# Kernel tuning notes

Measured on AMD Instinct MI355X. Metric: run time of the kernel, lower is better.

## Reference

```python
import jax, jax.numpy as jnp
import numpy as np

N, E, B = 50000, 400000, 64
N_INC, E_OUTC, U_INC, G_INC = 64, 64, 32, 64
H1A, H1B = 128, 64           # node_model_mlp1_hidden_sizes
H2 = 256                     # node_model_mlp2_hidden_sizes[0]
DIM_LH, DIM_L, N_OUTC = 128, 32, 64
LN_EPS = 1e-5

def _lin_init(key, din, dout):
    k1, k2 = jax.random.split(key)
    bound = 1.0 / np.sqrt(din)
    W = jax.random.uniform(k1, (din, dout), jnp.float32, -bound, bound)
    b = jax.random.uniform(k2, (dout,), jnp.float32, -bound, bound)
    return W, b

def setup_inputs() -> dict:
    key = jax.random.key(0)
    ks = jax.random.split(key, 16)
    x = jax.random.normal(ks[0], (N, N_INC), jnp.float32)
    edge_index = jax.random.randint(ks[1], (2, E), 0, N, jnp.int64)
    edge_attr = jax.random.normal(ks[2], (E, E_OUTC), jnp.float32)
    u = jax.random.normal(ks[3], (B, U_INC), jnp.float32)
    batch = jnp.sort(jax.random.randint(ks[4], (N,), 0, B, jnp.int64))
    goal = jax.random.normal(ks[5], (N, G_INC), jnp.float32)
    W1, b1 = _lin_init(ks[6], N_INC + E_OUTC, H1A)
    g1, be1 = jnp.ones((H1A,), jnp.float32), jnp.zeros((H1A,), jnp.float32)
    W2, b2 = _lin_init(ks[7], H1A, H1B)
    mlp2_inc = N_INC + H1B + U_INC
    W3, b3 = _lin_init(ks[8], mlp2_inc, H2)
    g3, be3 = jnp.ones((H2,), jnp.float32), jnp.zeros((H2,), jnp.float32)
    W4, b4 = _lin_init(ks[9], H2, DIM_LH)
    g4, be4 = jnp.ones((DIM_LH,), jnp.float32), jnp.zeros((DIM_LH,), jnp.float32)
    Wm, bm = _lin_init(ks[10], DIM_LH, DIM_L)
    Wv, bv = _lin_init(ks[11], DIM_LH, DIM_L)
    Wx, bx = _lin_init(ks[12], DIM_L, N_OUTC)
    return dict(x=x, edge_index=edge_index, edge_attr=edge_attr, u=u, batch=batch,
                goal=goal, W1=W1, b1=b1, g1=g1, be1=be1, W2=W2, b2=b2,
                W3=W3, b3=b3, g3=g3, be3=be3, W4=W4, b4=b4, g4=g4, be4=be4,
                Wm=Wm, bm=bm, Wv=Wv, bv=bv, Wx=Wx, bx=bx)

def _layernorm(h, g, b):
    mu = jnp.mean(h, axis=-1, keepdims=True)
    var = jnp.var(h, axis=-1, keepdims=True)
    return (h - mu) * jax.lax.rsqrt(var + LN_EPS) * g + b

def reference(x, edge_index, edge_attr, u, batch, goal,
              W1, b1, g1, be1, W2, b2,
              W3, b3, g3, be3, W4, b4, g4, be4,
              Wm, bm, Wv, bv, Wx, bx):
    row, col = edge_index[0], edge_index[1]
    # --- edge MLP: gather x[row], concat edge_attr, 2-layer MLP with LN+ReLU
    se = jnp.concatenate([x[row], edge_attr], axis=1)          # [E, n_inc+e_outc]
    h = jax.nn.relu(_layernorm(se @ W1 + b1, g1, be1)) @ W2 + b2  # [E, H1B]
    # --- scatter_mean over destination nodes
    sums = jax.ops.segment_sum(h, col, num_segments=N)          # [N, H1B]
    cnts = jax.ops.segment_sum(jnp.ones((E,), h.dtype), col, num_segments=N)
    aggs = sums / jnp.maximum(cnts, 1.0)[:, None]
    # --- node MLP 2
    z = jnp.concatenate([x, aggs, u[batch]], axis=1)            # [N, mlp2_inc]
    z = jax.nn.relu(_layernorm(z @ W3 + b3, g3, be3))
    z = jax.nn.relu(_layernorm(z @ W4 + b4, g4, be4))           # [N, DIM_LH]
    z_mu = z @ Wm + bm
    z_var = z @ Wv + bv                                         # log-variance
    eps = jax.random.normal(jax.random.key(42), z_mu.shape, z_mu.dtype)
    z_s = z_mu + eps * jnp.exp(0.5 * z_var)                     # reparameterize
    out = z_s @ Wx + bx                                         # [N, n_outc]
    return (out, z_mu, z_var)
```

## Files before the change

### kernel.cpp

```cpp
#include <hip/hip_runtime.h>

#define NN 50000
#define EE 400000
#define NB 49

typedef __attribute__((ext_vector_type(8))) short bf16x8;
typedef __attribute__((ext_vector_type(4))) float f32x4;

__device__ __forceinline__ void fma4(float4& a, float s, const float4& w){
  a.x = fmaf(s, w.x, a.x);
  a.y = fmaf(s, w.y, a.y);
  a.z = fmaf(s, w.z, a.z);
  a.w = fmaf(s, w.w, a.w);
}

__device__ __forceinline__ unsigned short f2bf(float f){
  unsigned u = __float_as_uint(f);
  unsigned r = (u + 0x7fffu + ((u >> 16) & 1u)) >> 16;
  return (unsigned short)r;
}

__device__ __forceinline__ bf16x8 cvt8(float4 lo, float4 hi){
  bf16x8 r;
  r[0]=(short)f2bf(lo.x); r[1]=(short)f2bf(lo.y); r[2]=(short)f2bf(lo.z); r[3]=(short)f2bf(lo.w);
  r[4]=(short)f2bf(hi.x); r[5]=(short)f2bf(hi.y); r[6]=(short)f2bf(hi.z); r[7]=(short)f2bf(hi.w);
  return r;
}

__device__ __forceinline__ unsigned packhl(float v){
  unsigned hi = f2bf(v);
  float fh = __uint_as_float(hi << 16);
  unsigned lo = f2bf(v - fh);
  return (hi << 16) | lo;
}

__device__ __forceinline__ uint4 pack4(float4 v){
  uint4 p;
  p.x = packhl(v.x); p.y = packhl(v.y); p.z = packhl(v.z); p.w = packhl(v.w);
  return p;
}

__device__ __forceinline__ void unpack8(uint4 p0, uint4 p1, bf16x8& hi, bf16x8& lo){
  hi[0]=(short)(p0.x>>16); lo[0]=(short)(p0.x & 0xffffu);
  hi[1]=(short)(p0.y>>16); lo[1]=(short)(p0.y & 0xffffu);
  hi[2]=(short)(p0.z>>16); lo[2]=(short)(p0.z & 0xffffu);
  hi[3]=(short)(p0.w>>16); lo[3]=(short)(p0.w & 0xffffu);
  hi[4]=(short)(p1.x>>16); lo[4]=(short)(p1.x & 0xffffu);
  hi[5]=(short)(p1.y>>16); lo[5]=(short)(p1.y & 0xffffu);
  hi[6]=(short)(p1.z>>16); lo[6]=(short)(p1.z & 0xffffu);
  hi[7]=(short)(p1.w>>16); lo[7]=(short)(p1.w & 0xffffu);
}

__device__ __forceinline__ float blo(unsigned u){ return __uint_as_float(u << 16); }
__device__ __forceinline__ float bhi(unsigned u){ return __uint_as_float(u & 0xffff0000u); }

__device__ __forceinline__ unsigned rotl32(unsigned v, int d){ return (v<<d)|(v>>(32-d)); }

__device__ __forceinline__ float eps_at(unsigned idx){
  const unsigned k0 = 0u, k1 = 42u, k2 = 0x1BD11BDAu ^ 0u ^ 42u;
  unsigned x0 = 0u + k0, x1 = idx + k1;
  const int rotA[4] = {13,15,26,6};
  const int rotB[4] = {17,29,16,24};
  #pragma unroll
  for (int i=0;i<4;i++){ x0 += x1; x1 = rotl32(x1, rotA[i]); x1 ^= x0; }
  x0 += k1; x1 += k2 + 1u;
  #pragma unroll
  for (int i=0;i<4;i++){ x0 += x1; x1 = rotl32(x1, rotB[i]); x1 ^= x0; }
  x0 += k2; x1 += k0 + 2u;
  #pragma unroll
  for (int i=0;i<4;i++){ x0 += x1; x1 = rotl32(x1, rotA[i]); x1 ^= x0; }
  x0 += k0; x1 += k1 + 3u;
  #pragma unroll
  for (int i=0;i<4;i++){ x0 += x1; x1 = rotl32(x1, rotB[i]); x1 ^= x0; }
  x0 += k1; x1 += k2 + 4u;
  #pragma unroll
  for (int i=0;i<4;i++){ x0 += x1; x1 = rotl32(x1, rotA[i]); x1 ^= x0; }
  x0 += k2; x1 += k0 + 5u;
  unsigned bits = x0 ^ x1;
  float f = __uint_as_float((bits >> 9) | 0x3f800000u) - 1.0f;
  const float lo = -0.99999994f;
  float u = f * 2.0f + lo;
  u = fmaxf(u, lo);
  float w = -log1pf(-u*u);
  float p;
  if (w < 5.0f){
    w -= 2.5f;
    p = 2.81022636e-08f;
    p = fmaf(p,w, 3.43273939e-07f);
    p = fmaf(p,w,-3.5233877e-06f);
    p = fmaf(p,w,-4.39150654e-06f);
    p = fmaf(p,w, 0.00021858087f);
    p = fmaf(p,w,-0.00125372503f);
    p = fmaf(p,w,-0.00417768164f);
    p = fmaf(p,w, 0.246640727f);
    p = fmaf(p,w, 1.50140941f);
  } else {
    w = sqrtf(w) - 3.0f;
    p = -0.000200214257f;
    p = fmaf(p,w, 0.000100950558f);
    p = fmaf(p,w, 0.00134934322f);
    p = fmaf(p,w,-0.00367342844f);
    p = fmaf(p,w, 0.00573950773f);
    p = fmaf(p,w,-0.0076224613f);
    p = fmaf(p,w, 0.00943887047f);
    p = fmaf(p,w, 1.00167406f);
    p = fmaf(p,w, 2.83297682f);
  }
  return 1.41421356237f * (p * u);
}

__global__ __launch_bounds__(256) void k_prep_x(const float* __restrict__ x,
                                                unsigned short* __restrict__ xb){
  int t = blockIdx.x*256 + threadIdx.x;
  if (t < NN*64/8){
    const float4* p = (const float4*)(x + t*8);
    bf16x8 v = cvt8(p[0], p[1]);
    *(bf16x8*)(xb + t*8) = v;
  }
}

__global__ __launch_bounds__(256) void k_prep_w(const float* __restrict__ W1,
                                                const float* __restrict__ W2,
                                                unsigned short* __restrict__ W1T,
                                                unsigned short* __restrict__ W2T){
  for (int i = threadIdx.x; i < 128*128; i += 256){
    int n = i >> 7, k = i & 127;
    W1T[i] = f2bf(W1[k*128 + n]);
  }
  for (int i = threadIdx.x; i < 64*128; i += 256){
    int n = i >> 7, k = i & 127;
    W2T[i] = f2bf(W2[k*64 + n]);
  }
}

__global__ __launch_bounds__(256) void k_prep_w34(const float* __restrict__ W3,
                                                  const float* __restrict__ W4,
                                                  unsigned short* __restrict__ W3Th,
                                                  unsigned short* __restrict__ W3Tl,
                                                  unsigned short* __restrict__ W4Th,
                                                  unsigned short* __restrict__ W4Tl){
  int b = blockIdx.x;
  if (b < 256){
    int n = b;
    for (int k = threadIdx.x; k < 160; k += 256){
      float w = W3[k*256 + n];
      unsigned h = f2bf(w);
      float fh = __uint_as_float(h << 16);
      W3Th[n*160 + k] = (unsigned short)h;
      W3Tl[n*160 + k] = f2bf(w - fh);
    }
  } else {
    int n = b - 256;
    int k = threadIdx.x;
    float w = W4[k*128 + n];
    unsigned h = f2bf(w);
    float fh = __uint_as_float(h << 16);
    W4Th[n*256 + k] = (unsigned short)h;
    W4Tl[n*256 + k] = f2bf(w - fh);
  }
}

__global__ __launch_bounds__(256) void k_hist(const int* __restrict__ ei, int* __restrict__ cnt){
  int e = blockIdx.x*256 + threadIdx.x;
  if (e < EE) atomicAdd(&cnt[ei[EE + e]], 1);
}

__global__ __launch_bounds__(256) void k_scan1(const int* __restrict__ cnt,
                                               int* __restrict__ offs,
                                               int* __restrict__ partials){
  __shared__ int sdata[256];
  const int t = threadIdx.x, b = blockIdx.x;
  const int base = b*1024 + t*4;
  int v0 = (base+0 < NN) ? cnt[base+0] : 0;
  int v1 = (base+1 < NN) ? cnt[base+1] : 0;
  int v2 = (base+2 < NN) ? cnt[base+2] : 0;
  int v3 = (base+3 < NN) ? cnt[base+3] : 0;
  int tsum = v0+v1+v2+v3;
  sdata[t] = tsum;
  __syncthreads();
  for (int off=1; off<256; off<<=1){
    int add = (t >= off) ? sdata[t-off] : 0;
    __syncthreads();
    sdata[t] += add;
    __syncthreads();
  }
  int run = sdata[t] - tsum;
  if (base+0 < NN) offs[base+0] = run;  run += v0;
  if (base+1 < NN) offs[base+1] = run;  run += v1;
  if (base+2 < NN) offs[base+2] = run;  run += v2;
  if (base+3 < NN) offs[base+3] = run;
  if (t == 255) partials[b] = sdata[255];
}

__global__ __launch_bounds__(64) void k_scan2(int* __restrict__ partials){
  int l = threadIdx.x;
  int v = (l < NB) ? partials[l] : 0;
  int inc = v;
  #pragma unroll
  for (int off=1; off<64; off<<=1){
    int t = __shfl_up(inc, off);
    if (l >= off) inc += t;
  }
  if (l < NB) partials[l] = inc - v;
}

__global__ __launch_bounds__(256) void k_scan3(int* __restrict__ offs,
                                               const int* __restrict__ partials,
                                               int* __restrict__ cursor){
  const int t = threadIdx.x, b = blockIdx.x;
  const int base = b*1024 + t*4;
  int add = partials[b];
  #pragma unroll
  for (int k=0;k<4;k++){
    int i = base + k;
    if (i < NN){ int o = offs[i] + add; offs[i] = o; cursor[i] = o; }
  }
}

__global__ __launch_bounds__(256) void k_fill(const int* __restrict__ ei,
                                              int* __restrict__ cursor,
                                              int* __restrict__ epos){
  int e = blockIdx.x*256 + threadIdx.x;
  if (e < EE){
    int c = ei[EE + e];
    epos[e] = atomicAdd(&cursor[c], 1);
  }
}

#define H1STR 132
__global__ __launch_bounds__(256, 4) void k_edge(const int* __restrict__ ei,
    const float* __restrict__ ea,
    const unsigned short* __restrict__ xb,
    const unsigned short* __restrict__ W1T, const float* __restrict__ b1,
    const float* __restrict__ g1, const float* __restrict__ be1,
    const unsigned short* __restrict__ W2T, const float* __restrict__ b2,
    const int* __restrict__ epos,
    unsigned short* __restrict__ h_ws){
  __shared__ __align__(16) float h1[64*H1STR];
  __shared__ int rows_l[64];
  __shared__ int slot_l[64];
  const int tid  = threadIdx.x;
  const int base = blockIdx.x * 64;
  const int wv   = tid >> 6;
  const int lane = tid & 63;
  const int quad = lane >> 4;
  const int l16  = lane & 15;
  if (tid < 64) rows_l[tid] = ei[base + tid];
  if (tid >= 128 && tid < 192) slot_l[tid-128] = epos[base + tid - 128];
  __syncthreads();
  {
    int rw[4];
    #pragma unroll
    for (int m=0;m<4;m++) rw[m] = rows_l[m*16 + l16];
    f32x4 acc[4][2];
    #pragma unroll
    for (int m=0;m<4;m++){ acc[m][0] = (f32x4){0.f,0.f,0.f,0.f}; acc[m][1] = (f32x4){0.f,0.f,0.f,0.f}; }
    #pragma unroll
    for (int ks=0; ks<4; ks++){
      bf16x8 af[4];
      if (ks < 2){
        #pragma unroll
        for (int m=0;m<4;m++)
          af[m] = *(const bf16x8*)(xb + (size_t)rw[m]*64 + ks*32 + quad*8);
      } else {
        #pragma unroll
        for (int m=0;m<4;m++){
          const float* p = ea + (size_t)(base + m*16 + l16)*64 + (ks-2)*32 + quad*8;
          af[m] = cvt8(*(const float4*)p, *(const float4*)(p+4));
        }
      }
      bf16x8 bf0 = *(const bf16x8*)(W1T + (size_t)((2*wv+0)*16 + l16)*128 + ks*32 + quad*8);
      bf16x8 bf1 = *(const bf16x8*)(W1T + (size_t)((2*wv+1)*16 + l16)*128 + ks*32 + quad*8);
      #pragma unroll
      for (int m=0;m<4;m++){
        acc[m][0] = __builtin_amdgcn_mfma_f32_16x16x32_bf16(af[m], bf0, acc[m][0], 0, 0, 0);
        acc[m][1] = __builtin_amdgcn_mfma_f32_16x16x32_bf16(af[m], bf1, acc[m][1], 0, 0, 0);
      }
    }
    #pragma unroll
    for (int nl=0; nl<2; nl++){
      float b1c = b1[(2*wv+nl)*16 + l16];
      #pragma unroll
      for (int m=0;m<4;m++){
        #pragma unroll
        for (int r=0;r<4;r++)
          h1[(m*16 + quad*4 + r)*H1STR + (2*wv+nl)*16 + l16] = acc[m][nl][r] + b1c;
      }
    }
  }
  __syncthreads();
  {
    const float gA = g1[lane], gB = g1[lane+64];
    const float bA = be1[lane], bB = be1[lane+64];
    for (int r = wv*16; r < wv*16 + 16; ++r){
      float a = h1[r*H1STR + lane];
      float b = h1[r*H1STR + 64 + lane];
      float s = a + b, ss = fmaf(a,a,b*b);
      #pragma unroll
      for (int off=32; off; off>>=1){
        s  += __shfl_xor(s, off);
        ss += __shfl_xor(ss, off);
      }
      float mean = s * (1.0f/128.0f);
      float var  = ss * (1.0f/128.0f) - mean*mean;
      float inv = rsqrtf(var + 1e-5f);
      h1[r*H1STR + lane]      = fmaxf(fmaf((a-mean)*inv, gA, bA), 0.f);
      h1[r*H1STR + 64 + lane] = fmaxf(fmaf((b-mean)*inv, gB, bB), 0.f);
    }
  }
  __syncthreads();
  {
    f32x4 acc2[4];
    #pragma unroll
    for (int m=0;m<4;m++) acc2[m] = (f32x4){0.f,0.f,0.f,0.f};
    #pragma unroll
    for (int ks=0; ks<4; ks++){
      bf16x8 bfr = *(const bf16x8*)(W2T + (size_t)(wv*16 + l16)*128 + ks*32 + quad*8);
      #pragma unroll
      for (int m=0;m<4;m++){
        const float* p = h1 + (m*16 + l16)*H1STR + ks*32 + quad*8;
        bf16x8 af = cvt8(*(const float4*)p, *(const float4*)(p+4));
        acc2[m] = __builtin_amdgcn_mfma_f32_16x16x32_bf16(af, bfr, acc2[m], 0, 0, 0);
      }
    }
    float b2c = b2[wv*16 + l16];
    #pragma unroll
    for (int m=0;m<4;m++){
      #pragma unroll
      for (int r=0;r<4;r++)
        h_ws[(size_t)slot_l[m*16 + quad*4 + r]*64 + wv*16 + l16] = f2bf(acc2[m][r] + b2c);
    }
  }
}

__global__ __launch_bounds__(256, 8) void k_agg(const float* __restrict__ x,
    const float* __restrict__ u, const int* __restrict__ batch,
    const unsigned short* __restrict__ h_ws, const int* __restrict__ cnt,
    const int* __restrict__ offs, unsigned* __restrict__ zg){
  int t = blockIdx.x*256 + threadIdx.x;
  int n = t >> 3, p = t & 7;
  if (n >= NN) return;
  unsigned* zr = zg + (size_t)n*160;
  {
    const float4* xp = (const float4*)(x + (size_t)n*64 + p*8);
    *(uint4*)(zr + p*8)     = pack4(xp[0]);
    *(uint4*)(zr + p*8 + 4) = pack4(xp[1]);
  }
  {
    const float4* up = (const float4*)(u + (size_t)batch[n]*32 + p*4);
    *(uint4*)(zr + 128 + p*4) = pack4(up[0]);
  }
  float a0=0.f,a1=0.f,a2=0.f,a3=0.f,a4=0.f,a5=0.f,a6=0.f,a7=0.f;
  int deg = cnt[n];
  const unsigned short* hp = h_ws + (size_t)offs[n]*64 + p*8;
  int j = 0;
  for (; j + 4 <= deg; j += 4){
    uint4 v0 = *(const uint4*)(hp);
    uint4 v1 = *(const uint4*)(hp + 64);
    uint4 v2 = *(const uint4*)(hp + 128);
    uint4 v3 = *(const uint4*)(hp + 192);
    hp += 256;
    a0 += blo(v0.x); a1 += bhi(v0.x); a2 += blo(v0.y); a3 += bhi(v0.y);
    a4 += blo(v0.z); a5 += bhi(v0.z); a6 += blo(v0.w); a7 += bhi(v0.w);
    a0 += blo(v1.x); a1 += bhi(v1.x); a2 += blo(v1.y); a3 += bhi(v1.y);
    a4 += blo(v1.z); a5 += bhi(v1.z); a6 += blo(v1.w); a7 += bhi(v1.w);
    a0 += blo(v2.x); a1 += bhi(v2.x); a2 += blo(v2.y); a3 += bhi(v2.y);
    a4 += blo(v2.z); a5 += bhi(v2.z); a6 += blo(v2.w); a7 += bhi(v2.w);
    a0 += blo(v3.x); a1 += bhi(v3.x); a2 += blo(v3.y); a3 += bhi(v3.y);
    a4 += blo(v3.z); a5 += bhi(v3.z); a6 += blo(v3.w); a7 += bhi(v3.w);
  }
  for (; j < deg; ++j){
    uint4 v = *(const uint4*)(hp);
    hp += 64;
    a0 += blo(v.x); a1 += bhi(v.x); a2 += blo(v.y); a3 += bhi(v.y);
    a4 += blo(v.z); a5 += bhi(v.z); a6 += blo(v.w); a7 += bhi(v.w);
  }
  float rc = 1.0f / fmaxf((float)deg, 1.0f);
  *(uint4*)(zr + 64 + p*8)     = pack4(make_float4(a0*rc, a1*rc, a2*rc, a3*rc));
  *(uint4*)(zr + 64 + p*8 + 4) = pack4(make_float4(a4*rc, a5*rc, a6*rc, a7*rc));
}

#define T2STR 132
#define ZSSTR 36
#define H3STR 260
__global__ __launch_bounds__(128, 3) void k_node(const unsigned* __restrict__ zg,
    const unsigned short* __restrict__ W3Th, const unsigned short* __restrict__ W3Tl,
    const float* __restrict__ b3,
    const float* __restrict__ g3, const float* __restrict__ be3,
    const unsigned short* __restrict__ W4Th, const unsigned short* __restrict__ W4Tl,
    const float* __restrict__ b4,
    const float* __restrict__ g4, const float* __restrict__ be4,
    const float* __restrict__ Wm, const float* __restrict__ bm,
    const float* __restrict__ Wv, const float* __restrict__ bv,
    const float* __restrict__ Wx, const float* __restrict__ bx,
    float* __restrict__ out){
  __shared__ __align__(16) char arena[(16*H3STR + 16*T2STR)*4];
  float*    h3f = (float*)arena;
  unsigned* h3p = (unsigned*)arena;
  float*    t2S = (float*)(arena + 16*H3STR*4);

  const int tid = threadIdx.x;
  const int base = blockIdx.x * 16;
  const int wv   = tid >> 6;
  const int lane = tid & 63;
  const int quad = lane >> 4;
  const int l16  = lane & 15;

  {
    const unsigned* az = zg + (size_t)(base + l16)*160 + quad*8;
    f32x4 acc[8];
    #pragma unroll
    for (int i=0;i<8;i++) acc[i] = (f32x4){0.f,0.f,0.f,0.f};
    #pragma unroll
    for (int ks=0; ks<5; ks++){
      uint4 p0 = *(const uint4*)(az + ks*32);
      uint4 p1 = *(const uint4*)(az + ks*32 + 4);
      bf16x8 ah, al;
      unpack8(p0, p1, ah, al);
      #pragma unroll
      for (int i=0;i<8;i++){
        int nt = wv*8 + i;
        bf16x8 bh = *(const bf16x8*)(W3Th + (size_t)(nt*16 + l16)*160 + ks*32 + quad*8);
        bf16x8 bl = *(const bf16x8*)(W3Tl + (size_t)(nt*16 + l16)*160 + ks*32 + quad*8);
        acc[i] = __builtin_amdgcn_mfma_f32_16x16x32_bf16(ah, bh, acc[i], 0, 0, 0);
        acc[i] = __builtin_amdgcn_mfma_f32_16x16x32_bf16(al, bh, acc[i], 0, 0, 0);
        acc[i] = __builtin_amdgcn_mfma_f32_16x16x32_bf16(ah, bl, acc[i], 0, 0, 0);
      }
    }
    #pragma unroll
    for (int i=0;i<8;i++){
      int nt = wv*8 + i;
      float bc = b3[nt*16 + l16];
      #pragma unroll
      for (int r=0;r<4;r++)
        h3f[(quad*4 + r)*H3STR + nt*16 + l16] = acc[i][r] + bc;
    }
  }
  __syncthreads();
  {
    float4 gg  = *(const float4*)(g3 + lane*4);
    float4 bet = *(const float4*)(be3 + lane*4);
    #pragma unroll
    for (int r=0;r<8;r++){
      int row = wv*8 + r;
      float4 v = *(const float4*)(h3f + row*H3STR + lane*4);
      float s  = v.x + v.y + v.z + v.w;
      float ss = fmaf(v.x,v.x, fmaf(v.y,v.y, fmaf(v.z,v.z, v.w*v.w)));
      #pragma unroll
      for (int off=32; off; off>>=1){ s += __shfl_xor(s,off); ss += __shfl_xor(ss,off); }
      float mean = s * (1.0f/256.0f);
      float inv  = rsqrtf(ss*(1.0f/256.0f) - mean*mean + 1e-5f);
      float4 o;
      o.x = fmaxf(fmaf((v.x-mean)*inv, gg.x, bet.x), 0.f);
      o.y = fmaxf(fmaf((v.y-mean)*inv, gg.y, bet.y), 0.f);
      o.z = fmaxf(fmaf((v.z-mean)*inv, gg.z, bet.z), 0.f);
      o.w = fmaxf(fmaf((v.w-mean)*inv, gg.w, bet.w), 0.f);
      *(uint4*)(h3p + row*H3STR + lane*4) = pack4(o);
    }
  }
  __syncthreads();
  {
    f32x4 acc[4];
    #pragma unroll
    for (int i=0;i<4;i++) acc[i] = (f32x4){0.f,0.f,0.f,0.f};
    #pragma unroll
    for (int ks=0; ks<8; ks++){
      const unsigned* ap = h3p + l16*H3STR + ks*32 + quad*8;
      uint4 p0 = *(const uint4*)ap;
      uint4 p1 = *(const uint4*)(ap + 4);
      bf16x8 ah, al;
      unpack8(p0, p1, ah, al);
      #pragma unroll
      for (int i=0;i<4;i++){
        int nt = wv*4 + i;
        bf16x8 bh = *(const bf16x8*)(W4Th + (size_t)(nt*16 + l16)*256 + ks*32 + quad*8);
        bf16x8 bl = *(const bf16x8*)(W4Tl + (size_t)(nt*16 + l16)*256 + ks*32 + quad*8);
        acc[i] = __builtin_amdgcn_mfma_f32_16x16x32_bf16(ah, bh, acc[i], 0, 0, 0);
        acc[i] = __builtin_amdgcn_mfma_f32_16x16x32_bf16(al, bh, acc[i], 0, 0, 0);
        acc[i] = __builtin_amdgcn_mfma_f32_16x16x32_bf16(ah, bl, acc[i], 0, 0, 0);
      }
    }
    #pragma unroll
    for (int i=0;i<4;i++){
      int nt = wv*4 + i;
      float bc = b4[nt*16 + l16];
      #pragma unroll
      for (int r=0;r<4;r++)
        t2S[(quad*4 + r)*T2STR + nt*16 + l16] = acc[i][r] + bc;
    }
  }
  __syncthreads();
  {
    const int jq = tid & 31, rb = tid >> 5;
    float4 gg  = *(const float4*)(g4 + 4*jq);
    float4 bet = *(const float4*)(be4 + 4*jq);
    #pragma unroll
    for (int r=0;r<4;r++){
      int row = rb*4 + r;
      float4 v = *(const float4*)(t2S + row*T2STR + 4*jq);
      float s  = v.x + v.y + v.z + v.w;
      float ss = fmaf(v.x,v.x, fmaf(v.y,v.y, fmaf(v.z,v.z, v.w*v.w)));
      #pragma unroll
      for (int off=16; off; off>>=1){ s += __shfl_xor(s,off); ss += __shfl_xor(ss,off); }
      float mean = s * (1.0f/128.0f);
      float inv  = rsqrtf(ss*(1.0f/128.0f) - mean*mean + 1e-5f);
      float4 o;
      o.x = fmaxf(fmaf((v.x-mean)*inv, gg.x, bet.x), 0.f);
      o.y = fmaxf(fmaf((v.y-mean)*inv, gg.y, bet.y), 0.f);
      o.z = fmaxf(fmaf((v.z-mean)*inv, gg.z, bet.z), 0.f);
      o.w = fmaxf(fmaf((v.w-mean)*inv, gg.w, bet.w), 0.f);
      *(float4*)(t2S + row*T2STR + 4*jq) = o;
    }
  }
  __syncthreads();
  {
    const int jq = tid & 15, rb = tid >> 4;
    const float* Wp = (jq < 8) ? Wm : Wv;
    const int cq = (jq & 7) * 4;
    float4 acc[2];
    #pragma unroll
    for (int r=0;r<2;r++) acc[r] = make_float4(0.f,0.f,0.f,0.f);
    #pragma unroll 2
    for (int k=0;k<128;k+=4){
      float4 w0 = *(const float4*)(Wp + (k+0)*32 + cq);
      float4 w1 = *(const float4*)(Wp + (k+1)*32 + cq);
      float4 w2 = *(const float4*)(Wp + (k+2)*32 + cq);
      float4 w3 = *(const float4*)(Wp + (k+3)*32 + cq);
      #pragma unroll
      for (int r=0;r<2;r++){
        float4 z = *(const float4*)(t2S + (rb*2+r)*T2STR + k);
        fma4(acc[r], z.x, w0); fma4(acc[r], z.y, w1);
        fma4(acc[r], z.z, w2); fma4(acc[r], z.w, w3);
      }
    }
    const float* bp = (jq < 8) ? bm : bv;
    float4 bb = *(const float4*)(bp + cq);
    const long long sec = (jq < 8) ? (long long)NN*64 : ((long long)NN*64 + (long long)NN*32);
    #pragma unroll
    for (int r=0;r<2;r++){
      float4 v = acc[r];
      v.x += bb.x; v.y += bb.y; v.z += bb.z; v.w += bb.w;
      int rr = rb*2 + r;
      *(float4*)(h3f + rr*64 + ((jq<8)?0:32) + cq) = v;
      int n = base + rr;
      if (n < NN) *(float4*)(out + sec + (long long)n*32 + cq) = v;
    }
  }
  __syncthreads();
  #pragma unroll
  for (int i=0;i<4;i++){
    int l = tid + 128*i;
    int r = l >> 5, jj = l & 31;
    float mu = h3f[r*64 + jj];
    float lv = h3f[r*64 + 32 + jj];
    unsigned idx = (unsigned)((base + r)*32 + jj);
    float e = eps_at(idx);
    t2S[r*ZSSTR + jj] = fmaf(e, expf(0.5f*lv), mu);
  }
  __syncthreads();
  {
    const int jq = tid & 15, rb = tid >> 4;
    float4 acc[2];
    #pragma unroll
    for (int r=0;r<2;r++) acc[r] = make_float4(0.f,0.f,0.f,0.f);
    #pragma unroll
    for (int k=0;k<32;k+=4){
      float4 w0 = *(const float4*)(Wx + (k+0)*64 + 4*jq);
      float4 w1 = *(const float4*)(Wx + (k+1)*64 + 4*jq);
      float4 w2 = *(const float4*)(Wx + (k+2)*64 + 4*jq);
      float4 w3 = *(const float4*)(Wx + (k+3)*64 + 4*jq);
      #pragma unroll
      for (int r=0;r<2;r++){
        float4 z = *(const float4*)(t2S + (rb*2+r)*ZSSTR + k);
        fma4(acc[r], z.x, w0); fma4(acc[r], z.y, w1);
        fma4(acc[r], z.z, w2); fma4(acc[r], z.w, w3);
      }
    }
    float4 bb = *(const float4*)(bx + 4*jq);
    #pragma unroll
    for (int r=0;r<2;r++){
      int n = base + rb*2 + r;
      if (n < NN){
        float4 v = acc[r];
        v.x += bb.x; v.y += bb.y; v.z += bb.z; v.w += bb.w;
        *(float4*)(out + (long long)n*64 + 4*jq) = v;
      }
    }
  }
}

extern "C" void kernel_launch(void* const* d_in, const int* in_sizes, int n_in,
                              void* d_out, int out_size, void* d_ws, size_t ws_size,
                              hipStream_t stream) {
  const float* x     = (const float*)d_in[0];
  const int*   ei    = (const int*)d_in[1];
  const float* ea    = (const float*)d_in[2];
  const float* u     = (const float*)d_in[3];
  const int*   batch = (const int*)d_in[4];
  const float* W1 = (const float*)d_in[6];
  const float* b1 = (const float*)d_in[7];
  const float* g1 = (const float*)d_in[8];
  const float* be1= (const float*)d_in[9];
  const float* W2 = (const float*)d_in[10];
  const float* b2 = (const float*)d_in[11];
  const float* W3 = (const float*)d_in[12];
  const float* b3 = (const float*)d_in[13];
  const float* g3 = (const float*)d_in[14];
  const float* be3= (const float*)d_in[15];
  const float* W4 = (const float*)d_in[16];
  const float* b4 = (const float*)d_in[17];
  const float* g4 = (const float*)d_in[18];
  const float* be4= (const float*)d_in[19];
  const float* Wm = (const float*)d_in[20];
  const float* bm = (const float*)d_in[21];
  const float* Wv = (const float*)d_in[22];
  const float* bv = (const float*)d_in[23];
  const float* Wx = (const float*)d_in[24];
  const float* bx = (const float*)d_in[25];

  char* W = (char*)d_ws;
  size_t off = 0;
  unsigned short* h_ws = (unsigned short*)(W + off); off += (size_t)EE*64*2;
  int* cnt      = (int*)(W + off);  off += (size_t)NN*4;
  int* offs     = (int*)(W + off);  off += (size_t)NN*4;
  int* cursor   = (int*)(W + off);  off += (size_t)NN*4;
  int* epos     = (int*)(W + off);  off += (size_t)EE*4;
  int* partials = (int*)(W + off);  off += 256;
  unsigned short* xb  = (unsigned short*)(W + off); off += (size_t)NN*64*2;
  unsigned short* W1T = (unsigned short*)(W + off); off += 128*128*2;
  unsigned short* W2T = (unsigned short*)(W + off); off += 64*128*2;
  unsigned short* W3Th = (unsigned short*)(W + off); off += 256*160*2;
  unsigned short* W3Tl = (unsigned short*)(W + off); off += 256*160*2;
  unsigned short* W4Th = (unsigned short*)(W + off); off += 128*256*2;
  unsigned short* W4Tl = (unsigned short*)(W + off); off += 128*256*2;
  off = (off + 255) & ~(size_t)255;
  unsigned* zg = (unsigned*)(W + off); off += (size_t)(NN + 32)*160*4;
  float* out = (float*)d_out;

  hipMemsetAsync(cnt, 0, (size_t)NN*sizeof(int), stream);

  k_prep_x<<<(NN*64/8 + 255)/256, 256, 0, stream>>>(x, xb);
  k_prep_w<<<1, 256, 0, stream>>>(W1, W2, W1T, W2T);
  k_prep_w34<<<384, 256, 0, stream>>>(W3, W4, W3Th, W3Tl, W4Th, W4Tl);
  k_hist <<<(EE+255)/256, 256, 0, stream>>>(ei, cnt);
  k_scan1<<<NB, 256, 0, stream>>>(cnt, offs, partials);
  k_scan2<<<1, 64, 0, stream>>>(partials);
  k_scan3<<<NB, 256, 0, stream>>>(offs, partials, cursor);
  k_fill <<<(EE+255)/256, 256, 0, stream>>>(ei, cursor, epos);

  k_edge<<<EE/64, 256, 0, stream>>>(ei, ea, xb, W1T, b1, g1, be1, W2T, b2, epos, h_ws);
  k_agg <<<(NN*8 + 255)/256, 256, 0, stream>>>(x, u, batch, h_ws, cnt, offs, zg);
  k_node<<<(NN+15)/16, 128, 0, stream>>>(zg,
                                         W3Th, W3Tl, b3, g3, be3,
                                         W4Th, W4Tl, b4, g4, be4,
                                         Wm,bm, Wv,bv, Wx,bx, out);
}
```

Before: 551.6 us.

## Tile k_node over 64 nodes per block with 4 waves reusing weight fragments

The node MLP kernel now handles 64 nodes per 256-thread block instead of 16 nodes per 128-thread block. Each wave computes four 16-row M tiles against fewer N tiles, so every W3/W4 bf16 fragment loaded from global memory feeds four MFMA row tiles instead of one. This cuts weight traffic per node. In exchange the kernel uses more registers for accumulators and much more LDS per block (about 66KB), which lowers occupancy. The shared arena is reused across stages with an extra barrier, and the zg workspace padding is enlarged to cover the bigger tiles.

```diff
diff --git a/kernel.cpp b/kernel.cpp
--- a/kernel.cpp
+++ b/kernel.cpp
@@ -383,7 +383,7 @@
 #define T2STR 132
 #define ZSSTR 36
 #define H3STR 260
-__global__ __launch_bounds__(128, 3) void k_node(const unsigned* __restrict__ zg,
+__global__ __launch_bounds__(256, 2) void k_node(const unsigned* __restrict__ zg,
     const unsigned short* __restrict__ W3Th, const unsigned short* __restrict__ W3Tl,
     const float* __restrict__ b3,
     const float* __restrict__ g3, const float* __restrict__ be3,
@@ -394,46 +394,58 @@
     const float* __restrict__ Wv, const float* __restrict__ bv,
     const float* __restrict__ Wx, const float* __restrict__ bx,
     float* __restrict__ out){
-  __shared__ __align__(16) char arena[(16*H3STR + 16*T2STR)*4];
+  __shared__ __align__(16) char arena[64*H3STR*4];
   float*    h3f = (float*)arena;
   unsigned* h3p = (unsigned*)arena;
-  float*    t2S = (float*)(arena + 16*H3STR*4);
+  float*    t2S = (float*)arena;
+  float*    hmS = (float*)(arena + 33792);
+  float*    zsS = (float*)(arena + 50176);
 
   const int tid = threadIdx.x;
-  const int base = blockIdx.x * 16;
+  const int base = blockIdx.x * 64;
   const int wv   = tid >> 6;
   const int lane = tid & 63;
   const int quad = lane >> 4;
   const int l16  = lane & 15;
 
   {
-    const unsigned* az = zg + (size_t)(base + l16)*160 + quad*8;
-    f32x4 acc[8];
-    #pragma unroll
-    for (int i=0;i<8;i++) acc[i] = (f32x4){0.f,0.f,0.f,0.f};
+    f32x4 acc[4][4];
+    #pragma unroll
+    for (int m=0;m<4;m++)
+      #pragma unroll
+      for (int i=0;i<4;i++) acc[m][i] = (f32x4){0.f,0.f,0.f,0.f};
     #pragma unroll
     for (int ks=0; ks<5; ks++){
-      uint4 p0 = *(const uint4*)(az + ks*32);
-      uint4 p1 = *(const uint4*)(az + ks*32 + 4);
-      bf16x8 ah, al;
-      unpack8(p0, p1, ah, al);
-      #pragma unroll
-      for (int i=0;i<8;i++){
-        int nt = wv*8 + i;
+      bf16x8 ah[4], al[4];
+      #pragma unroll
+      for (int m=0;m<4;m++){
+        const unsigned* az = zg + (size_t)(base + m*16 + l16)*160 + ks*32 + quad*8;
+        uint4 p0 = *(const uint4*)az;
+        uint4 p1 = *(const uint4*)(az + 4);
+        unpack8(p0, p1, ah[m], al[m]);
+      }
+      #pragma unroll
+      for (int i=0;i<4;i++){
+        int nt = wv*4 + i;
         bf16x8 bh = *(const bf16x8*)(W3Th + (size_t)(nt*16 + l16)*160 + ks*32 + quad*8);
         bf16x8 bl = *(const bf16x8*)(W3Tl + (size_t)(nt*16 + l16)*160 + ks*32 + quad*8);
-        acc[i] = __builtin_amdgcn_mfma_f32_16x16x32_bf16(ah, bh, acc[i], 0, 0, 0);
-        acc[i] = __builtin_amdgcn_mfma_f32_16x16x32_bf16(al, bh, acc[i], 0, 0, 0);
-        acc[i] = __builtin_amdgcn_mfma_f32_16x16x32_bf16(ah, bl, acc[i], 0, 0, 0);
-      }
-    }
-    #pragma unroll
-    for (int i=0;i<8;i++){
-      int nt = wv*8 + i;
+        #pragma unroll
+        for (int m=0;m<4;m++){
+          acc[m][i] = __builtin_amdgcn_mfma_f32_16x16x32_bf16(ah[m], bh, acc[m][i], 0, 0, 0);
+          acc[m][i] = __builtin_amdgcn_mfma_f32_16x16x32_bf16(al[m], bh, acc[m][i], 0, 0, 0);
+          acc[m][i] = __builtin_amdgcn_mfma_f32_16x16x32_bf16(ah[m], bl, acc[m][i], 0, 0, 0);
+        }
+      }
+    }
+    #pragma unroll
+    for (int i=0;i<4;i++){
+      int nt = wv*4 + i;
       float bc = b3[nt*16 + l16];
       #pragma unroll
-      for (int r=0;r<4;r++)
-        h3f[(quad*4 + r)*H3STR + nt*16 + l16] = acc[i][r] + bc;
+      for (int m=0;m<4;m++)
+        #pragma unroll
+        for (int r=0;r<4;r++)
+          h3f[(m*16 + quad*4 + r)*H3STR + nt*16 + l16] = acc[m][i][r] + bc;
     }
   }
   __syncthreads();
@@ -441,8 +453,8 @@
     float4 gg  = *(const float4*)(g3 + lane*4);
     float4 bet = *(const float4*)(be3 + lane*4);
     #pragma unroll
-    for (int r=0;r<8;r++){
-      int row = wv*8 + r;
+    for (int r=0;r<16;r++){
+      int row = wv*16 + r;
       float4 v = *(const float4*)(h3f + row*H3STR + lane*4);
       float s  = v.x + v.y + v.z + v.w;
       float ss = fmaf(v.x,v.x, fmaf(v.y,v.y, fmaf(v.z,v.z, v.w*v.w)));
@@ -460,33 +472,42 @@
   }
   __syncthreads();
   {
-    f32x4 acc[4];
-    #pragma unroll
-    for (int i=0;i<4;i++) acc[i] = (f32x4){0.f,0.f,0.f,0.f};
+    f32x4 acc2[4][2];
+    #pragma unroll
+    for (int m=0;m<4;m++){ acc2[m][0] = (f32x4){0.f,0.f,0.f,0.f}; acc2[m][1] = (f32x4){0.f,0.f,0.f,0.f}; }
     #pragma unroll
     for (int ks=0; ks<8; ks++){
-      const unsigned* ap = h3p + l16*H3STR + ks*32 + quad*8;
-      uint4 p0 = *(const uint4*)ap;
-      uint4 p1 = *(const uint4*)(ap + 4);
-      bf16x8 ah, al;
-      unpack8(p0, p1, ah, al);
-      #pragma unroll
-      for (int i=0;i<4;i++){
-        int nt = wv*4 + i;
+      bf16x8 ah[4], al[4];
+      #pragma unroll
+      for (int m=0;m<4;m++){
+        const unsigned* ap = h3p + (m*16 + l16)*H3STR + ks*32 + quad*8;
+        uint4 p0 = *(const uint4*)ap;
+        uint4 p1 = *(const uint4*)(ap + 4);
+        unpack8(p0, p1, ah[m], al[m]);
+      }
+      #pragma unroll
+      for (int i=0;i<2;i++){
+        int nt = wv*2 + i;
         bf16x8 bh = *(const bf16x8*)(W4Th + (size_t)(nt*16 + l16)*256 + ks*32 + quad*8);
         bf16x8 bl = *(const bf16x8*)(W4Tl + (size_t)(nt*16 + l16)*256 + ks*32 + quad*8);
-        acc[i] = __builtin_amdgcn_mfma_f32_16x16x32_bf16(ah, bh, acc[i], 0, 0, 0);
-        acc[i] = __builtin_amdgcn_mfma_f32_16x16x32_bf16(al, bh, acc[i], 0, 0, 0);
-        acc[i] = __builtin_amdgcn_mfma_f32_16x16x32_bf16(ah, bl, acc[i], 0, 0, 0);
-      }
-    }
-    #pragma unroll
-    for (int i=0;i<4;i++){
-      int nt = wv*4 + i;
+        #pragma unroll
+        for (int m=0;m<4;m++){
+          acc2[m][i] = __builtin_amdgcn_mfma_f32_16x16x32_bf16(ah[m], bh, acc2[m][i], 0, 0, 0);
+          acc2[m][i] = __builtin_amdgcn_mfma_f32_16x16x32_bf16(al[m], bh, acc2[m][i], 0, 0, 0);
+          acc2[m][i] = __builtin_amdgcn_mfma_f32_16x16x32_bf16(ah[m], bl, acc2[m][i], 0, 0, 0);
+        }
+      }
+    }
+    __syncthreads();
+    #pragma unroll
+    for (int i=0;i<2;i++){
+      int nt = wv*2 + i;
       float bc = b4[nt*16 + l16];
       #pragma unroll
-      for (int r=0;r<4;r++)
-        t2S[(quad*4 + r)*T2STR + nt*16 + l16] = acc[i][r] + bc;
+      for (int m=0;m<4;m++)
+        #pragma unroll
+        for (int r=0;r<4;r++)
+          t2S[(m*16 + quad*4 + r)*T2STR + nt*16 + l16] = acc2[m][i][r] + bc;
     }
   }
   __syncthreads();
@@ -495,8 +516,8 @@
     float4 gg  = *(const float4*)(g4 + 4*jq);
     float4 bet = *(const float4*)(be4 + 4*jq);
     #pragma unroll
-    for (int r=0;r<4;r++){
-      int row = rb*4 + r;
+    for (int r=0;r<8;r++){
+      int row = rb*8 + r;
       float4 v = *(const float4*)(t2S + row*T2STR + 4*jq);
       float s  = v.x + v.y + v.z + v.w;
       float ss = fmaf(v.x,v.x, fmaf(v.y,v.y, fmaf(v.z,v.z, v.w*v.w)));
@@ -517,9 +538,9 @@
     const int jq = tid & 15, rb = tid >> 4;
     const float* Wp = (jq < 8) ? Wm : Wv;
     const int cq = (jq & 7) * 4;
-    float4 acc[2];
-    #pragma unroll
-    for (int r=0;r<2;r++) acc[r] = make_float4(0.f,0.f,0.f,0.f);
+    float4 acc[4];
+    #pragma unroll
+    for (int r=0;r<4;r++) acc[r] = make_float4(0.f,0.f,0.f,0.f);
     #pragma unroll 2
     for (int k=0;k<128;k+=4){
       float4 w0 = *(const float4*)(Wp + (k+0)*32 + cq);
@@ -527,8 +548,8 @@
       float4 w2 = *(const float4*)(Wp + (k+2)*32 + cq);
       float4 w3 = *(const float4*)(Wp + (k+3)*32 + cq);
       #pragma unroll
-      for (int r=0;r<2;r++){
-        float4 z = *(const float4*)(t2S + (rb*2+r)*T2STR + k);
+      for (int r=0;r<4;r++){
+        float4 z = *(const float4*)(t2S + (rb*4+r)*T2STR + k);
         fma4(acc[r], z.x, w0); fma4(acc[r], z.y, w1);
         fma4(acc[r], z.z, w2); fma4(acc[r], z.w, w3);
       }
@@ -537,32 +558,32 @@
     float4 bb = *(const float4*)(bp + cq);
     const long long sec = (jq < 8) ? (long long)NN*64 : ((long long)NN*64 + (long long)NN*32);
     #pragma unroll
-    for (int r=0;r<2;r++){
+    for (int r=0;r<4;r++){
       float4 v = acc[r];
       v.x += bb.x; v.y += bb.y; v.z += bb.z; v.w += bb.w;
-      int rr = rb*2 + r;
-      *(float4*)(h3f + rr*64 + ((jq<8)?0:32) + cq) = v;
+      int rr = rb*4 + r;
+      *(float4*)(hmS + rr*64 + ((jq<8)?0:32) + cq) = v;
       int n = base + rr;
       if (n < NN) *(float4*)(out + sec + (long long)n*32 + cq) = v;
     }
   }
   __syncthreads();
   #pragma unroll
-  for (int i=0;i<4;i++){
-    int l = tid + 128*i;
+  for (int i=0;i<8;i++){
+    int l = tid + 256*i;
     int r = l >> 5, jj = l & 31;
-    float mu = h3f[r*64 + jj];
-    float lv = h3f[r*64 + 32 + jj];
+    float mu = hmS[r*64 + jj];
+    float lv = hmS[r*64 + 32 + jj];
     unsigned idx = (unsigned)((base + r)*32 + jj);
     float e = eps_at(idx);
-    t2S[r*ZSSTR + jj] = fmaf(e, expf(0.5f*lv), mu);
+    zsS[r*ZSSTR + jj] = fmaf(e, expf(0.5f*lv), mu);
   }
   __syncthreads();
   {
     const int jq = tid & 15, rb = tid >> 4;
-    float4 acc[2];
-    #pragma unroll
-    for (int r=0;r<2;r++) acc[r] = make_float4(0.f,0.f,0.f,0.f);
+    float4 acc[4];
+    #pragma unroll
+    for (int r=0;r<4;r++) acc[r] = make_float4(0.f,0.f,0.f,0.f);
     #pragma unroll
     for (int k=0;k<32;k+=4){
       float4 w0 = *(const float4*)(Wx + (k+0)*64 + 4*jq);
@@ -570,16 +591,16 @@
       float4 w2 = *(const float4*)(Wx + (k+2)*64 + 4*jq);
       float4 w3 = *(const float4*)(Wx + (k+3)*64 + 4*jq);
       #pragma unroll
-      for (int r=0;r<2;r++){
-        float4 z = *(const float4*)(t2S + (rb*2+r)*ZSSTR + k);
+      for (int r=0;r<4;r++){
+        float4 z = *(const float4*)(zsS + (rb*4+r)*ZSSTR + k);
         fma4(acc[r], z.x, w0); fma4(acc[r], z.y, w1);
         fma4(acc[r], z.z, w2); fma4(acc[r], z.w, w3);
       }
     }
     float4 bb = *(const float4*)(bx + 4*jq);
     #pragma unroll
-    for (int r=0;r<2;r++){
-      int n = base + rb*2 + r;
+    for (int r=0;r<4;r++){
+      int n = base + rb*4 + r;
       if (n < NN){
         float4 v = acc[r];
         v.x += bb.x; v.y += bb.y; v.z += bb.z; v.w += bb.w;
@@ -634,7 +655,7 @@
   unsigned short* W4Th = (unsigned short*)(W + off); off += 128*256*2;
   unsigned short* W4Tl = (unsigned short*)(W + off); off += 128*256*2;
   off = (off + 255) & ~(size_t)255;
-  unsigned* zg = (unsigned*)(W + off); off += (size_t)(NN + 32)*160*4;
+  unsigned* zg = (unsigned*)(W + off); off += (size_t)(NN + 64)*160*4;
   float* out = (float*)d_out;
 
   hipMemsetAsync(cnt, 0, (size_t)NN*sizeof(int), stream);
@@ -650,7 +671,7 @@
 
   k_edge<<<EE/64, 256, 0, stream>>>(ei, ea, xb, W1T, b1, g1, be1, W2T, b2, epos, h_ws);
   k_agg <<<(NN*8 + 255)/256, 256, 0, stream>>>(x, u, batch, h_ws, cnt, offs, zg);
-  k_node<<<(NN+15)/16, 128, 0, stream>>>(zg,
+  k_node<<<(NN+63)/64, 256, 0, stream>>>(zg,
                                          W3Th, W3Tl, b3, g3, be3,
                                          W4Th, W4Tl, b4, g4, be4,
                                          Wm,bm, Wv,bv, Wx,bx, out);
```

New measurement: 495.0 us. 10.3% less time.
